# Optimization experiments

Hardware: AMD Instinct MI355X
Metric: run time of the kernel (lower is better)

Reference implementation:

```python
import jax, jax.numpy as jnp
import numpy as np

IN_DIM = 768   # 256 + 256 + 128 + 128
OUT_DIM = 256
N_EDGES = 320000
N_GRAPHS = 64


def setup_inputs() -> dict:
    key = jax.random.key(0)
    ks = jax.random.split(key, 7)
    src = jax.random.normal(ks[0], (N_EDGES, 256), dtype=jnp.float32)
    dest = jax.random.normal(ks[1], (N_EDGES, 256), dtype=jnp.float32)
    edge_attr = jax.random.normal(ks[2], (N_EDGES, 128), dtype=jnp.float32)
    u = jax.random.normal(ks[3], (N_GRAPHS, 128), dtype=jnp.float32)
    batch = jnp.sort(jax.random.randint(ks[4], (N_EDGES,), 0, N_GRAPHS, dtype=jnp.int64)) if jax.config.read('jax_enable_x64') else jnp.sort(jax.random.randint(ks[4], (N_EDGES,), 0, N_GRAPHS)).astype(jnp.int32)
    # Linear(in_dim, out_dim): torch default init ~ U(-1/sqrt(in), 1/sqrt(in))
    bound = 1.0 / np.sqrt(IN_DIM)
    W = jax.random.uniform(ks[5], (IN_DIM, OUT_DIM), dtype=jnp.float32, minval=-bound, maxval=bound)
    b = jax.random.uniform(ks[6], (OUT_DIM,), dtype=jnp.float32, minval=-bound, maxval=bound)
    return {"src": src, "dest": dest, "edge_attr": edge_attr, "u": u, "batch": batch, "W": W, "b": b}


def reference(src, dest, edge_attr, u, batch, W, b):
    # u_expanded = u[batch]; concat [dest, src, edge_attr, u_exp]; Linear + ReLU
    u_exp = jnp.take(u, batch, axis=0)                    # [E, 128]
    combined = jnp.concatenate([dest, src, edge_attr, u_exp], axis=1)  # [E, 768]
    out = combined @ W + b                                # [E, 256]
    return jax.nn.relu(out)
```

## Files before the change

kernel.cpp:

```cpp
#include <hip/hip_runtime.h>
#include <cstdint>
#include <cstddef>

#define BM 64
#define BN 256
#define BK 32
#define NT 24
#define THREADS 512
#define A_BYTES (BM * BK * 2)
#define B_BYTES (BN * BK * 2)
#define BUF_BYTES (A_BYTES + B_BYTES)
#define NBUF 2

typedef __attribute__((ext_vector_type(4))) float f32x4;
typedef __attribute__((ext_vector_type(8))) short bf16x8;
typedef __attribute__((ext_vector_type(2))) unsigned int u32x2;

__device__ __forceinline__ unsigned int f2bf(float f) {
  union { float f; uint32_t u; } v; v.f = f;
  uint32_t r = v.u + 0x7FFFu + ((v.u >> 16) & 1u);
  return r >> 16;
}

__global__ void wt_kernel(const float* __restrict__ W, unsigned short* __restrict__ WtS) {
  const int gid = blockIdx.x * 256 + threadIdx.x;
  const int kt = gid >> 10;
  const int c  = gid & 1023;
  const int n  = ((c >> 6) << 4) | (c & 15);
  const int k0 = kt * 32 + ((c >> 4) & 3) * 8;
  unsigned int p[4];
#pragma unroll
  for (int i = 0; i < 4; ++i)
    p[i] = f2bf(W[(size_t)(k0 + 2 * i) * 256 + n]) |
           (f2bf(W[(size_t)(k0 + 2 * i + 1) * 256 + n]) << 16);
  *(u32x2*)((char*)WtS + (size_t)gid * 16)     = u32x2{p[0], p[1]};
  *(u32x2*)((char*)WtS + (size_t)gid * 16 + 8) = u32x2{p[2], p[3]};
}

__global__ __launch_bounds__(THREADS, 6) void edge_gemm(
    const float* __restrict__ srcf, const float* __restrict__ destf,
    const float* __restrict__ eaf, const float* __restrict__ uf,
    const int* __restrict__ batch, const unsigned short* __restrict__ WtS,
    const float* __restrict__ bias, float* __restrict__ out)
{
  __shared__ char smem[NBUF * BUF_BYTES];
  const int tid  = threadIdx.x;
  const int lane = tid & 63;
  const int w    = tid >> 6;
  const int wr   = w >> 2;
  const int wc   = w & 3;
  const int m0   = blockIdx.x * BM;
  const int l15  = lane & 15;
  const int l4   = lane >> 4;

  const int s_row  = ((tid >> 7) << 4) | ((tid >> 1) & 15);
  const int s_coff = (((tid >> 5) & 3) << 3) | ((tid & 1) << 2);
  const int s_ae   = m0 + s_row;
  const int s_ub   = batch[s_ae];

  float bs[4];
#pragma unroll
  for (int nf = 0; nf < 4; ++nf) bs[nf] = bias[wc * 64 + nf * 16 + l15];

  f32x4 acc[2][4];
  f32x4 z = {0.f, 0.f, 0.f, 0.f};
#pragma unroll
  for (int i = 0; i < 2; ++i)
#pragma unroll
    for (int j = 0; j < 4; ++j) acc[i][j] = z;

  auto a_ptr = [&](int kt) -> const float* {
    if (kt < 8)  return destf + (size_t)s_ae * 256 + kt * 32 + s_coff;
    if (kt < 16) return srcf  + (size_t)s_ae * 256 + (kt - 8) * 32 + s_coff;
    if (kt < 20) return eaf   + (size_t)s_ae * 128 + (kt - 16) * 32 + s_coff;
    return uf + (size_t)s_ub * 128 + (kt - 20) * 32 + s_coff;
  };

  f32x4 va;

  auto stage = [&](int kt) {
    char* Bb = smem + (kt & 1) * BUF_BYTES + A_BYTES;
    const char* wb = (const char*)WtS + (size_t)kt * B_BYTES;
#pragma unroll
    for (int j = 0; j < 2; ++j) {
      const char* g = wb + (size_t)(j * 512 + tid) * 16;
      char* l = Bb + (size_t)(j * 512 + w * 64) * 16;
      __builtin_amdgcn_global_load_lds(
          (const __attribute__((address_space(1))) uint32_t*)g,
          (__attribute__((address_space(3))) uint32_t*)l, 16, 0, 0);
    }
    va = *(const f32x4*)a_ptr(kt);
  };
  auto write_a = [&](int kt) {
    char* Ab = smem + (kt & 1) * BUF_BYTES;
    u32x2 p;
    p[0] = f2bf(va[0]) | (f2bf(va[1]) << 16);
    p[1] = f2bf(va[2]) | (f2bf(va[3]) << 16);
    *(u32x2*)(Ab + tid * 8) = p;
  };
  auto compute = [&](int kt) {
    const char* Ab = smem + (kt & 1) * BUF_BYTES;
    const char* Bb = Ab + A_BYTES;
    bf16x8 af[2], bfr[4];
#pragma unroll
    for (int mf = 0; mf < 2; ++mf)
      af[mf] = *(const bf16x8*)(Ab + (((wr * 2 + mf) * 64) + l4 * 16 + l15) * 16);
#pragma unroll
    for (int nf = 0; nf < 4; ++nf)
      bfr[nf] = *(const bf16x8*)(Bb + (((wc * 4 + nf) * 64) + l4 * 16 + l15) * 16);
#pragma unroll
    for (int mf = 0; mf < 2; ++mf)
#pragma unroll
      for (int nf = 0; nf < 4; ++nf)
        acc[mf][nf] = __builtin_amdgcn_mfma_f32_16x16x32_bf16(
            af[mf], bfr[nf], acc[mf][nf], 0, 0, 0);
  };

  stage(0);
  write_a(0);
  __syncthreads();

#pragma unroll
  for (int kt = 0; kt < NT; ++kt) {
    if (kt + 1 < NT) stage(kt + 1);
    compute(kt);
    if (kt + 1 < NT) write_a(kt + 1);
    __syncthreads();
  }

#pragma unroll
  for (int mf = 0; mf < 2; ++mf) {
    const int r0 = m0 + wr * 32 + mf * 16 + l4 * 4;
#pragma unroll
    for (int nf = 0; nf < 4; ++nf) {
      const int cn = wc * 64 + nf * 16 + l15;
      const f32x4 v = acc[mf][nf];
#pragma unroll
      for (int j = 0; j < 4; ++j) {
        const float x = v[j] + bs[nf];
        out[(size_t)(r0 + j) * 256 + cn] = x > 0.f ? x : 0.f;
      }
    }
  }
}

extern "C" void kernel_launch(void* const* d_in, const int* in_sizes, int n_in,
                              void* d_out, int out_size, void* d_ws, size_t ws_size,
                              hipStream_t stream) {
  const float* srcf  = (const float*)d_in[0];
  const float* destf = (const float*)d_in[1];
  const float* eaf   = (const float*)d_in[2];
  const float* uf    = (const float*)d_in[3];
  const int*   batch = (const int*)d_in[4];
  const float* W     = (const float*)d_in[5];
  const float* bias  = (const float*)d_in[6];
  float* out = (float*)d_out;
  unsigned short* WtS = (unsigned short*)d_ws;

  wt_kernel<<<96, 256, 0, stream>>>(W, WtS);

  edge_gemm<<<320000 / BM, THREADS, 0, stream>>>(
      srcf, destf, eaf, uf, batch, WtS, bias, out);
}
```

Baseline: 302.7 us.

## Load A fragments directly into registers, bypassing LDS, with explicit vmcnt pipelining

Each wave now reads its own A rows straight from global memory into registers and converts them to bf16 MFMA fragments, so the A tile no longer goes through LDS. The redundant per-wave A loads (wc=0..3 waves each load the same rows) trade LDS traffic and one sync stage for up to four times the global reads of A, served by cache. It adds a manual s_waitcnt vmcnt(4) with sched barriers so the A loads can stay in flight across the barrier, and lowers the launch-bounds occupancy hint from 6 to 4 to make room for the larger register footprint.

```diff
diff --git a/kernel.cpp b/kernel.cpp
--- a/kernel.cpp
+++ b/kernel.cpp
@@ -3,14 +3,9 @@
 #include <cstddef>
 
 #define BM 64
-#define BN 256
-#define BK 32
 #define NT 24
 #define THREADS 512
-#define A_BYTES (BM * BK * 2)
-#define B_BYTES (BN * BK * 2)
-#define BUF_BYTES (A_BYTES + B_BYTES)
-#define NBUF 2
+#define B_BYTES 16384
 
 typedef __attribute__((ext_vector_type(4))) float f32x4;
 typedef __attribute__((ext_vector_type(8))) short bf16x8;
@@ -37,13 +32,13 @@
   *(u32x2*)((char*)WtS + (size_t)gid * 16 + 8) = u32x2{p[2], p[3]};
 }
 
-__global__ __launch_bounds__(THREADS, 6) void edge_gemm(
+__global__ __launch_bounds__(THREADS, 4) void edge_gemm(
     const float* __restrict__ srcf, const float* __restrict__ destf,
     const float* __restrict__ eaf, const float* __restrict__ uf,
     const int* __restrict__ batch, const unsigned short* __restrict__ WtS,
     const float* __restrict__ bias, float* __restrict__ out)
 {
-  __shared__ char smem[NBUF * BUF_BYTES];
+  __shared__ char smem[2 * B_BYTES];
   const int tid  = threadIdx.x;
   const int lane = tid & 63;
   const int w    = tid >> 6;
@@ -53,10 +48,10 @@
   const int l15  = lane & 15;
   const int l4   = lane >> 4;
 
-  const int s_row  = ((tid >> 7) << 4) | ((tid >> 1) & 15);
-  const int s_coff = (((tid >> 5) & 3) << 3) | ((tid & 1) << 2);
-  const int s_ae   = m0 + s_row;
-  const int s_ub   = batch[s_ae];
+  const int arow0 = m0 + wr * 32 + l15;
+  const int arow1 = arow0 + 16;
+  const int ub0 = batch[arow0];
+  const int ub1 = batch[arow1];
 
   float bs[4];
 #pragma unroll
@@ -69,17 +64,26 @@
 #pragma unroll
     for (int j = 0; j < 4; ++j) acc[i][j] = z;
 
-  auto a_ptr = [&](int kt) -> const float* {
-    if (kt < 8)  return destf + (size_t)s_ae * 256 + kt * 32 + s_coff;
-    if (kt < 16) return srcf  + (size_t)s_ae * 256 + (kt - 8) * 32 + s_coff;
-    if (kt < 20) return eaf   + (size_t)s_ae * 128 + (kt - 16) * 32 + s_coff;
-    return uf + (size_t)s_ub * 128 + (kt - 20) * 32 + s_coff;
+  auto a_ptr = [&](int kt, int row, int ubr) -> const float* {
+    const int c = l4 * 8;
+    if (kt < 8)  return destf + (size_t)row * 256 + kt * 32 + c;
+    if (kt < 16) return srcf  + (size_t)row * 256 + (kt - 8) * 32 + c;
+    if (kt < 20) return eaf   + (size_t)row * 128 + (kt - 16) * 32 + c;
+    return uf + (size_t)ubr * 128 + (kt - 20) * 32 + c;
   };
 
-  f32x4 va;
+  f32x4 va[2][2][2];
 
-  auto stage = [&](int kt) {
-    char* Bb = smem + (kt & 1) * BUF_BYTES + A_BYTES;
+  auto loadA = [&](int kt) {
+    const float* p0 = a_ptr(kt, arow0, ub0);
+    const float* p1 = a_ptr(kt, arow1, ub1);
+    va[kt & 1][0][0] = *(const f32x4*)(p0);
+    va[kt & 1][0][1] = *(const f32x4*)(p0 + 4);
+    va[kt & 1][1][0] = *(const f32x4*)(p1);
+    va[kt & 1][1][1] = *(const f32x4*)(p1 + 4);
+  };
+  auto gldsB = [&](int kt) {
+    char* Bb = smem + (kt & 1) * B_BYTES;
     const char* wb = (const char*)WtS + (size_t)kt * B_BYTES;
 #pragma unroll
     for (int j = 0; j < 2; ++j) {
@@ -89,22 +93,37 @@
           (const __attribute__((address_space(1))) uint32_t*)g,
           (__attribute__((address_space(3))) uint32_t*)l, 16, 0, 0);
     }
-    va = *(const f32x4*)a_ptr(kt);
   };
-  auto write_a = [&](int kt) {
-    char* Ab = smem + (kt & 1) * BUF_BYTES;
-    u32x2 p;
-    p[0] = f2bf(va[0]) | (f2bf(va[1]) << 16);
-    p[1] = f2bf(va[2]) | (f2bf(va[3]) << 16);
-    *(u32x2*)(Ab + tid * 8) = p;
+  auto pack8 = [&](f32x4 a, f32x4 b) -> bf16x8 {
+    bf16x8 r;
+    r[0] = (short)f2bf(a[0]); r[1] = (short)f2bf(a[1]);
+    r[2] = (short)f2bf(a[2]); r[3] = (short)f2bf(a[3]);
+    r[4] = (short)f2bf(b[0]); r[5] = (short)f2bf(b[1]);
+    r[6] = (short)f2bf(b[2]); r[7] = (short)f2bf(b[3]);
+    return r;
   };
-  auto compute = [&](int kt) {
-    const char* Ab = smem + (kt & 1) * BUF_BYTES;
-    const char* Bb = Ab + A_BYTES;
-    bf16x8 af[2], bfr[4];
+
+  gldsB(0);
+  __builtin_amdgcn_sched_barrier(0);
+  loadA(0);
+  __builtin_amdgcn_sched_barrier(0);
+  asm volatile("s_waitcnt vmcnt(4)" ::: "memory");
+  __builtin_amdgcn_sched_barrier(0);
+  __builtin_amdgcn_s_barrier();
+
 #pragma unroll
-    for (int mf = 0; mf < 2; ++mf)
-      af[mf] = *(const bf16x8*)(Ab + (((wr * 2 + mf) * 64) + l4 * 16 + l15) * 16);
+  for (int kt = 0; kt < NT; ++kt) {
+    if (kt + 1 < NT) {
+      gldsB(kt + 1);
+      __builtin_amdgcn_sched_barrier(0);
+      loadA(kt + 1);
+      __builtin_amdgcn_sched_barrier(0);
+    }
+    bf16x8 af[2];
+    af[0] = pack8(va[kt & 1][0][0], va[kt & 1][0][1]);
+    af[1] = pack8(va[kt & 1][1][0], va[kt & 1][1][1]);
+    const char* Bb = smem + (kt & 1) * B_BYTES;
+    bf16x8 bfr[4];
 #pragma unroll
     for (int nf = 0; nf < 4; ++nf)
       bfr[nf] = *(const bf16x8*)(Bb + (((wc * 4 + nf) * 64) + l4 * 16 + l15) * 16);
@@ -114,18 +133,12 @@
       for (int nf = 0; nf < 4; ++nf)
         acc[mf][nf] = __builtin_amdgcn_mfma_f32_16x16x32_bf16(
             af[mf], bfr[nf], acc[mf][nf], 0, 0, 0);
-  };
-
-  stage(0);
-  write_a(0);
-  __syncthreads();
-
-#pragma unroll
-  for (int kt = 0; kt < NT; ++kt) {
-    if (kt + 1 < NT) stage(kt + 1);
-    compute(kt);
-    if (kt + 1 < NT) write_a(kt + 1);
-    __syncthreads();
+    if (kt + 1 < NT) {
+      __builtin_amdgcn_sched_barrier(0);
+      asm volatile("s_waitcnt vmcnt(4)" ::: "memory");
+      __builtin_amdgcn_sched_barrier(0);
+      __builtin_amdgcn_s_barrier();
+    }
   }
 
 #pragma unroll
```

Measured after the change: 506.7 us. +67.4%, slower.
